# Performance work log

Measured on AMD Instinct MI355X. Metric: run time of the kernel, lower is better.

Reference implementation:

```python
import jax, jax.numpy as jnp
import numpy as np

D_MODEL, D_KEY, N_HEADS = 256, 32, 8
B, T1, T2 = 4, 2048, 2048


def setup_inputs() -> dict:
    key = jax.random.key(0)
    ks = jax.random.split(key, 12)
    s = 1.0 / np.sqrt(D_MODEL)
    inp = {
        "key_input": jax.random.normal(ks[0], (B, T1, D_MODEL), jnp.float32),
        "query_input": jax.random.normal(ks[1], (B, T2, D_MODEL), jnp.float32),
        "value_input": jax.random.normal(ks[2], (B, T1, D_MODEL), jnp.float32),
        "attention_mask": jnp.ones((B, T1, T2), dtype=jnp.bool_),  # unused by the module, kept for API fidelity
        "WK_w": jax.random.uniform(ks[3], (D_KEY * N_HEADS, D_MODEL), jnp.float32, -s, s),
        "WK_b": jax.random.uniform(ks[4], (D_KEY * N_HEADS,), jnp.float32, -s, s),
        "WQ_w": jax.random.uniform(ks[5], (D_KEY * N_HEADS, D_MODEL), jnp.float32, -s, s),
        "WQ_b": jax.random.uniform(ks[6], (D_KEY * N_HEADS,), jnp.float32, -s, s),
        "WV_w": jax.random.uniform(ks[7], (D_MODEL * N_HEADS, D_MODEL), jnp.float32, -s, s),
        "WV_b": jax.random.uniform(ks[8], (D_MODEL * N_HEADS,), jnp.float32, -s, s),
        "WO_w": jax.random.uniform(ks[9], (D_MODEL, D_MODEL * N_HEADS), jnp.float32, -1.0 / np.sqrt(D_MODEL * N_HEADS), 1.0 / np.sqrt(D_MODEL * N_HEADS)),
        "WO_b": jax.random.uniform(ks[10], (D_MODEL,), jnp.float32, -1.0 / np.sqrt(D_MODEL * N_HEADS), 1.0 / np.sqrt(D_MODEL * N_HEADS)),
    }
    return inp


def reference(key_input, query_input, value_input, attention_mask,
              WK_w, WK_b, WQ_w, WQ_b, WV_w, WV_b, WO_w, WO_b):
    b, t1, dm = key_input.shape
    t2 = query_input.shape[1]
    h, dk = N_HEADS, D_KEY
    # projections
    k = key_input @ WK_w.T + WK_b      # [b, t1, h*dk]
    q = query_input @ WQ_w.T + WQ_b    # [b, t2, h*dk]
    v = value_input @ WV_w.T + WV_b    # [b, t1, h*dm] (per-head value dim == d_model)
    # head split: channel index c = head*dk + feat (head outer), matching torch reshapes
    k = k.reshape(b, t1, h, dk)
    q = q.reshape(b, t2, h, dk)
    v = v.reshape(b, t1, h, dm)
    # scores: NO 1/sqrt(dk) scaling and NO masking (faithful to source; mask arg unused)
    scores = jnp.einsum('bshk,bqhk->bhsq', k, q)      # [b, h, t1, t2]
    attn = jax.nn.softmax(scores, axis=2)             # softmax over KEY axis (torch dim=1 of [t1,t2])
    emb = jnp.einsum('bshd,bhsq->bqdh', v, attn)      # [b, t2, dm, h]
    emb = emb.reshape(b, t2, dm * h)                  # flatten (d_model outer, head inner)
    return emb @ WO_w.T + WO_b                        # [b, t2, d_model]
```

## Files before the change

kernel.cpp:

```cpp
#include <hip/hip_runtime.h>

typedef __attribute__((ext_vector_type(8))) short short8;
typedef __attribute__((ext_vector_type(4))) short short4v;
typedef __attribute__((ext_vector_type(4))) float float4v;
typedef __attribute__((ext_vector_type(4))) unsigned uint4v;
typedef __attribute__((ext_vector_type(2))) unsigned uint2v;

constexpr int T  = 2048;
constexpr int DM = 256;
constexpr int DK = 32;

__device__ inline short f2bf(float f) {
  unsigned u = __builtin_bit_cast(unsigned, f);
  u += 0x7fff + ((u >> 16) & 1);
  return (short)(u >> 16);
}

__device__ inline unsigned pk2(float a, float b) {
#if __has_builtin(__builtin_amdgcn_cvt_pk_bf16_f32)
  auto r = __builtin_amdgcn_cvt_pk_bf16_f32(a, b);
  return __builtin_bit_cast(unsigned, r);
#else
  unsigned ua = __builtin_bit_cast(unsigned, a);
  ua = (ua + 0x7fff + ((ua >> 16) & 1)) >> 16;
  unsigned ub = __builtin_bit_cast(unsigned, b);
  ub = (ub + 0x7fff + ((ub >> 16) & 1)) >> 16;
  return ua | (ub << 16);
#endif
}

__device__ inline float fexp2(float x) {
#if __has_builtin(__builtin_amdgcn_exp2f)
  return __builtin_amdgcn_exp2f(x);
#else
  return exp2f(x);
#endif
}

__device__ inline short8 load8_bf(const float* __restrict__ p) {
  float4v a = *(const float4v*)p;
  float4v b = *(const float4v*)(p + 4);
  uint4v u;
  u[0] = pk2(a[0], a[1]); u[1] = pk2(a[2], a[3]);
  u[2] = pk2(b[0], b[1]); u[3] = pk2(b[2], b[3]);
  return __builtin_bit_cast(short8, u);
}

__device__ inline void gemm_body64(const float* __restrict__ A,
                                   const float* __restrict__ Bw,
                                   const float* __restrict__ bias,
                                   short* __restrict__ C,
                                   float oscale, int bx, int by,
                                   int K, int N, int mode,
                                   short (&As)[128][40], short (&Bs)[64][40]) {
  const int tid  = threadIdx.x;
  const int wave = tid >> 6, lane = tid & 63;
  const int l15  = lane & 15, quad = lane >> 4;
  const int wm   = (wave & 1) * 64, wn = (wave >> 1) * 32;
  const long Abase = (long)bx * 128;
  const long Bbase = (long)by * 64;

  float4v acc[4][2];
  for (int i = 0; i < 4; i++)
    for (int j = 0; j < 2; j++)
      for (int r = 0; r < 4; r++) acc[i][j][r] = 0.f;

  const int srow = tid >> 2;
  const int sc8  = (tid & 3) * 8;

  for (int k0 = 0; k0 < K; k0 += 32) {
    __syncthreads();
    for (int i = 0; i < 2; i++) {
      int row = srow + i * 64;
      *(short8*)&As[row][sc8] = load8_bf(A + (Abase + row) * K + k0 + sc8);
    }
    *(short8*)&Bs[srow][sc8] = load8_bf(Bw + (Bbase + srow) * K + k0 + sc8);
    __syncthreads();
    short8 af[4], bfr[2];
    for (int ms = 0; ms < 4; ms++) af[ms]  = *(const short8*)&As[wm + ms*16 + l15][quad*8];
    for (int ns = 0; ns < 2; ns++) bfr[ns] = *(const short8*)&Bs[wn + ns*16 + l15][quad*8];
    for (int ms = 0; ms < 4; ms++)
      for (int ns = 0; ns < 2; ns++)
        acc[ms][ns] = __builtin_amdgcn_mfma_f32_16x16x32_bf16(af[ms], bfr[ns], acc[ms][ns], 0, 0, 0);
  }

  for (int ms = 0; ms < 4; ms++) {
    int rowl = wm + ms*16 + quad*4;
    for (int ns = 0; ns < 2; ns++) {
      int col = (int)Bbase + wn + ns*16 + l15;
      if (mode == 0) {
        float bv = bias[col];
        for (int r = 0; r < 4; r++) {
          long row = Abase + rowl + r;
          C[row * (long)N + col] = f2bf((acc[ms][ns][r] + bv) * oscale);
        }
      } else {
        int bidx = col >> 11, scol = col & 2047;
        for (int r = 0; r < 4; r++) {
          long m = Abase + rowl + r;
          C[((long)bidx * 2048 + m) * 2048 + scol] = f2bf(acc[ms][ns][r] + bias[m]);
        }
      }
    }
  }
}

__global__ __launch_bounds__(256)
void mega_proj(const float* __restrict__ key_x, const float* __restrict__ query_x,
               const float* __restrict__ value_x,
               const float* __restrict__ WK_w, const float* __restrict__ WK_b,
               const float* __restrict__ WQ_w, const float* __restrict__ WQ_b,
               const float* __restrict__ WV_w, const float* __restrict__ WV_b,
               const float* __restrict__ WO_w, const float* __restrict__ WO_b,
               short* __restrict__ Kp, short* __restrict__ Qp,
               short* __restrict__ Vt, short* __restrict__ WOpb,
               float* __restrict__ outp) {
  __shared__ __align__(16) short As[128][40];
  __shared__ __align__(16) short Bs[64][40];

  const int gb = blockIdx.x;
  if (gb < 512) {
    const int z  = gb >> 8;
    const int bx = gb & 63, by = (gb >> 6) & 3;
    const float L2E = 1.44269504f;
    if (z == 0)
      gemm_body64(key_x,   WK_w, WK_b, Kp, 1.0f, bx, by, 256, 256, 0, As, Bs);
    else
      gemm_body64(query_x, WQ_w, WQ_b, Qp, L2E,  bx, by, 256, 256, 0, As, Bs);
  } else if (gb < 2560) {
    const int sub = gb - 512;
    const int bx = sub & 15, by = sub >> 4;
    gemm_body64(WV_w, value_x, WV_b, Vt, 1.0f, bx, by, 256, 8192, 1, As, Bs);
  } else if (gb < 2624) {
    const int p = gb - 2560;
    for (int i = 0; i < 32; i++) {
      int idx = p * 8192 + i * 256 + threadIdx.x;
      int n = idx >> 11, c = idx & 2047;
      int h = c >> 8, d = c & 255;
      WOpb[idx] = f2bf(WO_w[n * 2048 + d * 8 + h]);
    }
  } else {
    const int p = gb - 2624;
    for (long i4 = ((long)p * 256 + threadIdx.x) * 4; i4 < 8192L * 256;
         i4 += 32L * 256 * 4) {
      float4v bv = *(const float4v*)(WO_b + (i4 & 255));
      *(float4v*)(outp + i4) = bv;
    }
  }
}

__global__ __launch_bounds__(256)
void gemm_sk(const short* __restrict__ A, const short* __restrict__ Bw,
             float* __restrict__ C) {
  __shared__ __align__(16) short As[128][40];
  __shared__ __align__(16) short Bs[64][40];

  const int tid  = threadIdx.x;
  const int wave = tid >> 6, lane = tid & 63;
  const int l15  = lane & 15, quad = lane >> 4;
  const int wm   = (wave & 1) * 64, wn = (wave >> 1) * 32;
  const long Abase = (long)blockIdx.x * 128;
  const long Bbase = (long)blockIdx.y * 64;
  const int  kbase = blockIdx.z * 1024;
  const int  N = 256, K = 2048;

  float4v acc[4][2];
  for (int i = 0; i < 4; i++)
    for (int j = 0; j < 2; j++)
      for (int r = 0; r < 4; r++) acc[i][j][r] = 0.f;

  const int srow = tid >> 2;
  const int sc8  = (tid & 3) * 8;

  for (int k0 = kbase; k0 < kbase + 1024; k0 += 32) {
    __syncthreads();
    for (int i = 0; i < 2; i++) {
      int row = srow + i * 64;
      *(short8*)&As[row][sc8] = *(const short8*)(A + (Abase + row) * K + k0 + sc8);
    }
    *(short8*)&Bs[srow][sc8] = *(const short8*)(Bw + (Bbase + srow) * K + k0 + sc8);
    __syncthreads();
    short8 af[4], bfr[2];
    for (int ms = 0; ms < 4; ms++) af[ms]  = *(const short8*)&As[wm + ms*16 + l15][quad*8];
    for (int ns = 0; ns < 2; ns++) bfr[ns] = *(const short8*)&Bs[wn + ns*16 + l15][quad*8];
    for (int ms = 0; ms < 4; ms++)
      for (int ns = 0; ns < 2; ns++)
        acc[ms][ns] = __builtin_amdgcn_mfma_f32_16x16x32_bf16(af[ms], bfr[ns], acc[ms][ns], 0, 0, 0);
  }

  for (int ms = 0; ms < 4; ms++) {
    int rowl = wm + ms*16 + quad*4;
    for (int ns = 0; ns < 2; ns++) {
      int col = (int)Bbase + wn + ns*16 + l15;
      for (int r = 0; r < 4; r++) {
        long row = Abase + rowl + r;
        atomicAdd(&C[row * (long)N + col], acc[ms][ns][r]);
      }
    }
  }
}

__global__ __launch_bounds__(256, 2)
void attn_kernel(const short* __restrict__ Kp, const short* __restrict__ Qp,
                 const short* __restrict__ Vt, short* __restrict__ emb) {
  __shared__ __align__(16) short Pt[2][128][136];
  __shared__ __align__(16) float psum[128][4];

  const int tid  = threadIdx.x;
  const int wave = tid >> 6, lane = tid & 63;
  const int l15  = lane & 15, quad = lane >> 4;

  const int L  = blockIdx.x;
  const int h  = L & 7;
  const int b  = (L >> 3) & 3;
  const int q0 = (L >> 5) * 128;

  const short* Kbh = Kp + (long)b * T * DM + h * DK;
  const short* Qbh = Qp + (long)b * T * DM + h * DK;
  const short* Vbh = Vt + ((long)b * 2048 + h * 256) * 2048;

  float4v acc[4][8];
  for (int i = 0; i < 4; i++)
    for (int j = 0; j < 8; j++)
      for (int r = 0; r < 4; r++) acc[i][j][r] = 0.f;

  float ps[8];
  for (int i = 0; i < 8; i++) ps[i] = 0.f;

  short8 qf[8];
  for (int qs = 0; qs < 8; qs++)
    qf[qs] = *(const short8*)(Qbh + (long)(q0 + qs*16 + l15) * DM + quad*8);

  auto computeSt = [&](int s0, int buf) {
    for (int ss = 0; ss < 2; ss++) {
      short8 kf = *(const short8*)(Kbh + (long)(s0 + wave*32 + ss*16 + l15) * DM + quad*8);
      for (int qs = 0; qs < 8; qs++) {
        float4v z = {0.f, 0.f, 0.f, 0.f};
        float4v st = __builtin_amdgcn_mfma_f32_16x16x32_bf16(kf, qf[qs], z, 0, 0, 0);
        float p0 = fexp2(st[0]), p1 = fexp2(st[1]);
        float p2 = fexp2(st[2]), p3 = fexp2(st[3]);
        ps[qs] += (p0 + p1) + (p2 + p3);
        uint2v pb; pb[0] = pk2(p0, p1); pb[1] = pk2(p2, p3);
        *(uint2v*)&Pt[buf][qs*16 + l15][wave*32 + ss*16 + quad*4] = pb;
      }
    }
  };

  computeSt(0, 0);

  for (int it = 0; it < T / 128; it++) {
    const int buf = it & 1;
    const int s0  = it * 128;
    __syncthreads();
    if (it < T / 128 - 1) computeSt(s0 + 128, buf ^ 1);
    for (int ks = 0; ks < 4; ks++) {
      short8 pf[8];
      for (int ns = 0; ns < 8; ns++)
        pf[ns] = *(const short8*)&Pt[buf][ns*16 + l15][ks*32 + quad*8];
      for (int ms = 0; ms < 4; ms++) {
        short8 vf = *(const short8*)(Vbh + (long)(wave*64 + ms*16 + l15) * 2048
                                     + s0 + ks*32 + quad*8);
        for (int ns = 0; ns < 8; ns++)
          acc[ms][ns] = __builtin_amdgcn_mfma_f32_16x16x32_bf16(vf, pf[ns], acc[ms][ns], 0, 0, 0);
      }
    }
  }

  for (int qs = 0; qs < 8; qs++) {
    ps[qs] += __shfl_xor(ps[qs], 16, 64);
    ps[qs] += __shfl_xor(ps[qs], 32, 64);
  }
  if (lane < 16)
    for (int qs = 0; qs < 8; qs++) psum[qs*16 + lane][wave] = ps[qs];
  __syncthreads();

  for (int ns = 0; ns < 8; ns++) {
    float4v sv = *(const float4v*)&psum[ns*16 + l15][0];
    float rl = 1.0f / (sv[0] + sv[1] + sv[2] + sv[3]);
    long rowbase = ((long)(b * T + q0 + ns*16 + l15)) * 2048 + h * 256;
    for (int ms = 0; ms < 4; ms++) {
      uint2v ob;
      ob[0] = pk2(acc[ms][ns][0] * rl, acc[ms][ns][1] * rl);
      ob[1] = pk2(acc[ms][ns][2] * rl, acc[ms][ns][3] * rl);
      *(uint2v*)(emb + rowbase + wave*64 + ms*16 + quad*4) = ob;
    }
  }
}

extern "C" void kernel_launch(void* const* d_in, const int* in_sizes, int n_in,
                              void* d_out, int out_size, void* d_ws, size_t ws_size,
                              hipStream_t stream) {
  const float* key_x   = (const float*)d_in[0];
  const float* query_x = (const float*)d_in[1];
  const float* value_x = (const float*)d_in[2];
  const float* WK_w = (const float*)d_in[4];
  const float* WK_b = (const float*)d_in[5];
  const float* WQ_w = (const float*)d_in[6];
  const float* WQ_b = (const float*)d_in[7];
  const float* WV_w = (const float*)d_in[8];
  const float* WV_b = (const float*)d_in[9];
  const float* WO_w = (const float*)d_in[10];
  const float* WO_b = (const float*)d_in[11];

  char* ws = (char*)d_ws;
  short* Kp   = (short*)(ws);
  short* Qp   = (short*)(ws + (4u  << 20));
  short* Vt   = (short*)(ws + (8u  << 20));
  short* embp = (short*)(ws + (40u << 20));
  short* WOpb = (short*)(ws + (72u << 20));
  float* outp = (float*)d_out;

  mega_proj<<<2656, 256, 0, stream>>>(key_x, query_x, value_x,
                                      WK_w, WK_b, WQ_w, WQ_b, WV_w, WV_b,
                                      WO_w, WO_b, Kp, Qp, Vt, WOpb, outp);
  attn_kernel<<<dim3(512), 256, 0, stream>>>(Kp, Qp, Vt, embp);
  gemm_sk<<<dim3(64, 4, 2), 256, 0, stream>>>(embp, WOpb, outp);
}
```

Before: 314.8 us.

## Fold output projection into value projection and accumulate attention output directly

Precomputes per-head fused weights WO_h·WV_h and a fused bias, projects value_input through them to get per-head 256-wide U tensors, and has the attention kernel atomically add normalized results plus bias into the final output. This removes the large emb intermediate write/read and the separate split-K output GEMM. In exchange it adds a small weight-fusion GEMM with strided scalar loads, eight-way atomic contention per output element, and extra bf16 rounding of the fused weights.

```diff
diff --git a/kernel.cpp b/kernel.cpp
--- a/kernel.cpp
+++ b/kernel.cpp
@@ -51,7 +51,7 @@
                                    const float* __restrict__ bias,
                                    short* __restrict__ C,
                                    float oscale, int bx, int by,
-                                   int K, int N, int mode,
+                                   int K, int N,
                                    short (&As)[128][40], short (&Bs)[64][40]) {
   const int tid  = threadIdx.x;
   const int wave = tid >> 6, lane = tid & 63;
@@ -88,70 +88,99 @@
     int rowl = wm + ms*16 + quad*4;
     for (int ns = 0; ns < 2; ns++) {
       int col = (int)Bbase + wn + ns*16 + l15;
-      if (mode == 0) {
-        float bv = bias[col];
-        for (int r = 0; r < 4; r++) {
-          long row = Abase + rowl + r;
-          C[row * (long)N + col] = f2bf((acc[ms][ns][r] + bv) * oscale);
-        }
-      } else {
-        int bidx = col >> 11, scol = col & 2047;
-        for (int r = 0; r < 4; r++) {
-          long m = Abase + rowl + r;
-          C[((long)bidx * 2048 + m) * 2048 + scol] = f2bf(acc[ms][ns][r] + bias[m]);
-        }
+      float bv = bias[col];
+      for (int r = 0; r < 4; r++) {
+        long row = Abase + rowl + r;
+        C[row * (long)N + col] = f2bf((acc[ms][ns][r] + bv) * oscale);
       }
     }
   }
 }
 
 __global__ __launch_bounds__(256)
-void mega_proj(const float* __restrict__ key_x, const float* __restrict__ query_x,
-               const float* __restrict__ value_x,
-               const float* __restrict__ WK_w, const float* __restrict__ WK_b,
-               const float* __restrict__ WQ_w, const float* __restrict__ WQ_b,
-               const float* __restrict__ WV_w, const float* __restrict__ WV_b,
-               const float* __restrict__ WO_w, const float* __restrict__ WO_b,
-               short* __restrict__ Kp, short* __restrict__ Qp,
-               short* __restrict__ Vt, short* __restrict__ WOpb,
-               float* __restrict__ outp) {
+void prep(const float* __restrict__ key_x, const float* __restrict__ query_x,
+          const float* __restrict__ WK_w, const float* __restrict__ WK_b,
+          const float* __restrict__ WQ_w, const float* __restrict__ WQ_b,
+          const float* __restrict__ WV_w, const float* __restrict__ WV_b,
+          const float* __restrict__ WO_w, const float* __restrict__ WO_b,
+          short* __restrict__ Kp, short* __restrict__ Qp,
+          short* __restrict__ Wf, float* __restrict__ cbias,
+          float* __restrict__ outp) {
   __shared__ __align__(16) short As[128][40];
   __shared__ __align__(16) short Bs[64][40];
 
-  const int gb = blockIdx.x;
+  const int gb  = blockIdx.x;
+  const int tid = threadIdx.x;
+
   if (gb < 512) {
-    const int z  = gb >> 8;
-    const int bx = gb & 63, by = (gb >> 6) & 3;
-    const float L2E = 1.44269504f;
-    if (z == 0)
-      gemm_body64(key_x,   WK_w, WK_b, Kp, 1.0f, bx, by, 256, 256, 0, As, Bs);
+    const int g = gb & 255;
+    const int bx = g & 63, by = g >> 6;
+    if (gb < 256)
+      gemm_body64(key_x,   WK_w, WK_b, Kp, 1.0f,        bx, by, 256, 256, As, Bs);
     else
-      gemm_body64(query_x, WQ_w, WQ_b, Qp, L2E,  bx, by, 256, 256, 0, As, Bs);
-  } else if (gb < 2560) {
-    const int sub = gb - 512;
-    const int bx = sub & 15, by = sub >> 4;
-    gemm_body64(WV_w, value_x, WV_b, Vt, 1.0f, bx, by, 256, 8192, 1, As, Bs);
-  } else if (gb < 2624) {
-    const int p = gb - 2560;
-    for (int i = 0; i < 32; i++) {
-      int idx = p * 8192 + i * 256 + threadIdx.x;
-      int n = idx >> 11, c = idx & 2047;
-      int h = c >> 8, d = c & 255;
-      WOpb[idx] = f2bf(WO_w[n * 2048 + d * 8 + h]);
-    }
+      gemm_body64(query_x, WQ_w, WQ_b, Qp, 1.44269504f, bx, by, 256, 256, As, Bs);
+  } else if (gb < 576) {
+    const int w  = gb - 512;
+    const int h  = w >> 3;
+    const int bx = (w >> 2) & 1;
+    const int by = w & 3;
+    const int wave = tid >> 6, lane = tid & 63;
+    const int l15  = lane & 15, quad = lane >> 4;
+    const int wm   = (wave & 1) * 64, wn = (wave >> 1) * 32;
+    const int srow = tid >> 2, sc8 = (tid & 3) * 8;
+
+    float4v acc[4][2];
+    for (int i = 0; i < 4; i++)
+      for (int j = 0; j < 2; j++)
+        for (int r = 0; r < 4; r++) acc[i][j][r] = 0.f;
+
+    for (int d0 = 0; d0 < 256; d0 += 32) {
+      __syncthreads();
+      for (int i = 0; i < 2; i++) {
+        int row = srow + i * 64;
+        for (int j = 0; j < 8; j++)
+          As[row][sc8 + j] = f2bf(WO_w[(bx*128 + row) * 2048 + (d0 + sc8 + j) * 8 + h]);
+      }
+      for (int j = 0; j < 8; j++)
+        Bs[srow][sc8 + j] = f2bf(WV_w[((h*256) + d0 + sc8 + j) * 256 + by*64 + srow]);
+      __syncthreads();
+      short8 af[4], bfr[2];
+      for (int ms = 0; ms < 4; ms++) af[ms]  = *(const short8*)&As[wm + ms*16 + l15][quad*8];
+      for (int ns = 0; ns < 2; ns++) bfr[ns] = *(const short8*)&Bs[wn + ns*16 + l15][quad*8];
+      for (int ms = 0; ms < 4; ms++)
+        for (int ns = 0; ns < 2; ns++)
+          acc[ms][ns] = __builtin_amdgcn_mfma_f32_16x16x32_bf16(af[ms], bfr[ns], acc[ms][ns], 0, 0, 0);
+    }
+    for (int ms = 0; ms < 4; ms++) {
+      int m = bx*128 + wm + ms*16 + quad*4;
+      for (int ns = 0; ns < 2; ns++) {
+        int col = by*64 + wn + ns*16 + l15;
+        for (int r = 0; r < 4; r++)
+          Wf[((long)h*256 + m + r) * 256 + col] = f2bf(acc[ms][ns][r]);
+      }
+    }
+  } else if (gb < 584) {
+    const int h = gb - 576;
+    const int n = tid;
+    float acc = 0.f;
+    for (int d = 0; d < 256; d++)
+      acc += WV_b[h*256 + d] * WO_w[n * 2048 + d*8 + h];
+    cbias[h*256 + n] = acc;
   } else {
-    const int p = gb - 2624;
-    for (long i4 = ((long)p * 256 + threadIdx.x) * 4; i4 < 8192L * 256;
-         i4 += 32L * 256 * 4) {
-      float4v bv = *(const float4v*)(WO_b + (i4 & 255));
-      *(float4v*)(outp + i4) = bv;
+    const int p  = gb - 584;
+    const int c4 = (tid & 63) * 4;
+    const int r0 = tid >> 6;
+    float4v bv = *(const float4v*)(WO_b + c4);
+    for (int i = 0; i < 64; i++) {
+      long row = (long)p*256 + r0*64 + i;
+      *(float4v*)(outp + row*256 + c4) = bv;
     }
   }
 }
 
 __global__ __launch_bounds__(256)
-void gemm_sk(const short* __restrict__ A, const short* __restrict__ Bw,
-             float* __restrict__ C) {
+void gemm_ut(const short* __restrict__ Wf, const float* __restrict__ Bw,
+             short* __restrict__ Ut) {
   __shared__ __align__(16) short As[128][40];
   __shared__ __align__(16) short Bs[64][40];
 
@@ -161,8 +190,6 @@
   const int wm   = (wave & 1) * 64, wn = (wave >> 1) * 32;
   const long Abase = (long)blockIdx.x * 128;
   const long Bbase = (long)blockIdx.y * 64;
-  const int  kbase = blockIdx.z * 1024;
-  const int  N = 256, K = 2048;
 
   float4v acc[4][2];
   for (int i = 0; i < 4; i++)
@@ -172,13 +199,13 @@
   const int srow = tid >> 2;
   const int sc8  = (tid & 3) * 8;
 
-  for (int k0 = kbase; k0 < kbase + 1024; k0 += 32) {
+  for (int k0 = 0; k0 < 256; k0 += 32) {
     __syncthreads();
     for (int i = 0; i < 2; i++) {
       int row = srow + i * 64;
-      *(short8*)&As[row][sc8] = *(const short8*)(A + (Abase + row) * K + k0 + sc8);
-    }
-    *(short8*)&Bs[srow][sc8] = *(const short8*)(Bw + (Bbase + srow) * K + k0 + sc8);
+      *(short8*)&As[row][sc8] = *(const short8*)(Wf + (Abase + row) * 256 + k0 + sc8);
+    }
+    *(short8*)&Bs[srow][sc8] = load8_bf(Bw + (Bbase + srow) * 256 + k0 + sc8);
     __syncthreads();
     short8 af[4], bfr[2];
     for (int ms = 0; ms < 4; ms++) af[ms]  = *(const short8*)&As[wm + ms*16 + l15][quad*8];
@@ -192,9 +219,10 @@
     int rowl = wm + ms*16 + quad*4;
     for (int ns = 0; ns < 2; ns++) {
       int col = (int)Bbase + wn + ns*16 + l15;
+      int bidx = col >> 11, scol = col & 2047;
       for (int r = 0; r < 4; r++) {
-        long row = Abase + rowl + r;
-        atomicAdd(&C[row * (long)N + col], acc[ms][ns][r]);
+        long m = Abase + rowl + r;
+        Ut[((long)bidx * 2048 + m) * 2048 + scol] = f2bf(acc[ms][ns][r]);
       }
     }
   }
@@ -202,7 +230,8 @@
 
 __global__ __launch_bounds__(256, 2)
 void attn_kernel(const short* __restrict__ Kp, const short* __restrict__ Qp,
-                 const short* __restrict__ Vt, short* __restrict__ emb) {
+                 const short* __restrict__ Ut, const float* __restrict__ cbias,
+                 float* __restrict__ outp) {
   __shared__ __align__(16) short Pt[2][128][136];
   __shared__ __align__(16) float psum[128][4];
 
@@ -217,7 +246,8 @@
 
   const short* Kbh = Kp + (long)b * T * DM + h * DK;
   const short* Qbh = Qp + (long)b * T * DM + h * DK;
-  const short* Vbh = Vt + ((long)b * 2048 + h * 256) * 2048;
+  const short* Ubh = Ut + ((long)b * 2048 + h * 256) * 2048;
+  const float* cb  = cbias + h * 256;
 
   float4v acc[4][8];
   for (int i = 0; i < 4; i++)
@@ -258,7 +288,7 @@
       for (int ns = 0; ns < 8; ns++)
         pf[ns] = *(const short8*)&Pt[buf][ns*16 + l15][ks*32 + quad*8];
       for (int ms = 0; ms < 4; ms++) {
-        short8 vf = *(const short8*)(Vbh + (long)(wave*64 + ms*16 + l15) * 2048
+        short8 vf = *(const short8*)(Ubh + (long)(wave*64 + ms*16 + l15) * 2048
                                      + s0 + ks*32 + quad*8);
         for (int ns = 0; ns < 8; ns++)
           acc[ms][ns] = __builtin_amdgcn_mfma_f32_16x16x32_bf16(vf, pf[ns], acc[ms][ns], 0, 0, 0);
@@ -277,12 +307,11 @@
   for (int ns = 0; ns < 8; ns++) {
     float4v sv = *(const float4v*)&psum[ns*16 + l15][0];
     float rl = 1.0f / (sv[0] + sv[1] + sv[2] + sv[3]);
-    long rowbase = ((long)(b * T + q0 + ns*16 + l15)) * 2048 + h * 256;
+    long rowbase = ((long)(b * T + q0 + ns*16 + l15)) * 256;
     for (int ms = 0; ms < 4; ms++) {
-      uint2v ob;
-      ob[0] = pk2(acc[ms][ns][0] * rl, acc[ms][ns][1] * rl);
-      ob[1] = pk2(acc[ms][ns][2] * rl, acc[ms][ns][3] * rl);
-      *(uint2v*)(emb + rowbase + wave*64 + ms*16 + quad*4) = ob;
+      int ncol = wave*64 + ms*16 + quad*4;
+      for (int r = 0; r < 4; r++)
+        atomicAdd(outp + rowbase + ncol + r, acc[ms][ns][r] * rl + cb[ncol + r]);
     }
   }
 }
@@ -303,16 +332,16 @@
   const float* WO_b = (const float*)d_in[11];
 
   char* ws = (char*)d_ws;
-  short* Kp   = (short*)(ws);
-  short* Qp   = (short*)(ws + (4u  << 20));
-  short* Vt   = (short*)(ws + (8u  << 20));
-  short* embp = (short*)(ws + (40u << 20));
-  short* WOpb = (short*)(ws + (72u << 20));
-  float* outp = (float*)d_out;
-
-  mega_proj<<<2656, 256, 0, stream>>>(key_x, query_x, value_x,
-                                      WK_w, WK_b, WQ_w, WQ_b, WV_w, WV_b,
-                                      WO_w, WO_b, Kp, Qp, Vt, WOpb, outp);
-  attn_kernel<<<dim3(512), 256, 0, stream>>>(Kp, Qp, Vt, embp);
-  gemm_sk<<<dim3(64, 4, 2), 256, 0, stream>>>(embp, WOpb, outp);
-}
+  short* Kp    = (short*)(ws);
+  short* Qp    = (short*)(ws + (4u  << 20));
+  short* Ut    = (short*)(ws + (8u  << 20));
+  short* Wf    = (short*)(ws + (40u << 20));
+  float* cbias = (float*)(ws + (41u << 20));
+  float* outp  = (float*)d_out;
+
+  prep<<<616, 256, 0, stream>>>(key_x, query_x, WK_w, WK_b, WQ_w, WQ_b,
+                                WV_w, WV_b, WO_w, WO_b,
+                                Kp, Qp, Wf, cbias, outp);
+  gemm_ut<<<dim3(16, 128), 256, 0, stream>>>(Wf, value_x, Ut);
+  attn_kernel<<<dim3(512), 256, 0, stream>>>(Kp, Qp, Ut, cbias, outp);
+}
```

Result: slower. 485.0 us (+54.1%).
